# Kernel optimization log

Hardware: AMD Instinct MI355X
Metric: run time of the kernel (lower is better)

Reference implementation:

```python
import jax, jax.numpy as jnp
import numpy as np

DIM = 1024
INTER = 1024
N_EXPERTS = 16
TOPK = 4
SHARED_INTER = 2 * INTER  # n_shared_experts * moe_inter_dim
T = 8192


def setup_inputs() -> dict:
    key = jax.random.key(0)
    ks = jax.random.split(key, 15)
    s = 0.02
    inp = {
        "x": jax.random.normal(ks[0], (T, DIM), jnp.float32),
        "gate_w": jax.random.normal(ks[1], (N_EXPERTS, DIM), jnp.float32) * s,
        # routed experts, stacked over expert axis
        "ew1": jax.random.normal(ks[2], (N_EXPERTS, INTER, DIM), jnp.float32) * s,
        "eb1": jax.random.normal(ks[3], (N_EXPERTS, INTER), jnp.float32) * s,
        "ew2": jax.random.normal(ks[4], (N_EXPERTS, DIM, INTER), jnp.float32) * s,
        "eb2": jax.random.normal(ks[5], (N_EXPERTS, DIM), jnp.float32) * s,
        "ew3": jax.random.normal(ks[6], (N_EXPERTS, INTER, DIM), jnp.float32) * s,
        "eb3": jax.random.normal(ks[7], (N_EXPERTS, INTER), jnp.float32) * s,
        # shared expert MLP (inter = 2 * moe_inter_dim)
        "sw1": jax.random.normal(ks[8], (SHARED_INTER, DIM), jnp.float32) * s,
        "sb1": jax.random.normal(ks[9], (SHARED_INTER,), jnp.float32) * s,
        "sw2": jax.random.normal(ks[10], (DIM, SHARED_INTER), jnp.float32) * s,
        "sb2": jax.random.normal(ks[11], (DIM,), jnp.float32) * s,
        "sw3": jax.random.normal(ks[12], (SHARED_INTER, DIM), jnp.float32) * s,
        "sb3": jax.random.normal(ks[13], (SHARED_INTER,), jnp.float32) * s,
    }
    return inp


def _ffn(x, w1, b1, w2, b2, w3, b3):
    # w2(silu(w1(x)) * w3(x))
    return (jax.nn.silu(x @ w1.T + b1) * (x @ w3.T + b3)) @ w2.T + b2


def reference(x, gate_w, ew1, eb1, ew2, eb2, ew3, eb3, sw1, sb1, sw2, sb2, sw3, sb3):
    # Gate: softmax scores in fp32 (n_groups=1 -> no group masking), top-k routing
    scores = jax.nn.softmax((x @ gate_w.T).astype(jnp.float32), axis=-1)  # [T, E]
    top_vals, idx = jax.lax.top_k(scores, TOPK)  # [T, K]
    weights = top_vals.astype(x.dtype)  # route_scale = 1.0, softmax score_func

    # Per-expert combine weight: zero for unselected experts.
    nT = x.shape[0]
    cw = jnp.zeros((nT, N_EXPERTS), x.dtype).at[
        jnp.arange(nT)[:, None], idx
    ].add(weights)  # [T, E]

    # Routed experts: masked-dense dispatch (weight 0 kills unselected terms)
    y = jnp.zeros_like(x)
    for e in range(N_EXPERTS):
        y = y + cw[:, e:e + 1] * _ffn(x, ew1[e], eb1[e], ew2[e], eb2[e], ew3[e], eb3[e])

    # Shared experts (always applied)
    z = _ffn(x, sw1, sb1, sw2, sb2, sw3, sb3)
    return y + z
```

## Files before the change

### kernel.cpp

```cpp
#include <hip/hip_runtime.h>
#include <cstdint>
#include <cstddef>

#define TOK     8192
#define DIMD    1024
#define INTERD  1024
#define NEXP    16
#define SINTER  2048
#define CAPROWS 34816
#define MAXTILES 272
#define HBLK    32

typedef __bf16 bf16_t;
typedef __bf16 bf16x8_t __attribute__((ext_vector_type(8)));
typedef __bf16 bf16x4_t __attribute__((ext_vector_type(4)));
typedef float  f32x4_t  __attribute__((ext_vector_type(4)));

__device__ __forceinline__ void gload_lds16(const bf16_t* g, bf16_t* l) {
  __builtin_amdgcn_global_load_lds((const __attribute__((address_space(1))) void*)g,
                                   (__attribute__((address_space(3))) void*)l,
                                   16, 0, 0);
}

__global__ void init_kernel(int* toklist, float* wtlist, int* tile_e, int* tile_rs) {
  int i = blockIdx.x * blockDim.x + threadIdx.x;
  if (i < CAPROWS) { toklist[i] = -1; wtlist[i] = 0.0f; }
  if (i < 512)     { tile_e[i] = -1; tile_rs[i] = 0; }
}

__global__ void cvt_kernel(const float* __restrict__ in, bf16_t* __restrict__ out, int n4) {
  int stride = gridDim.x * blockDim.x;
  for (int i = blockIdx.x * blockDim.x + threadIdx.x; i < n4; i += stride) {
    float4 v = ((const float4*)in)[i];
    bf16x4_t o;
    o[0] = (bf16_t)v.x; o[1] = (bf16_t)v.y; o[2] = (bf16_t)v.z; o[3] = (bf16_t)v.w;
    ((bf16x4_t*)out)[i] = o;
  }
}

__global__ __launch_bounds__(256)
void gate_kernel(const float* __restrict__ x, const float* __restrict__ gw,
                 int* __restrict__ tkidx, float* __restrict__ tkwt) {
  int wv = threadIdx.x >> 6, lane = threadIdx.x & 63;
  int t = blockIdx.x * 4 + wv;
  const float4* xp = (const float4*)(x + (size_t)t * DIMD + lane * 16);
  float4 xv[4];
#pragma unroll
  for (int i = 0; i < 4; ++i) xv[i] = xp[i];
  float sc[NEXP];
#pragma unroll
  for (int e = 0; e < NEXP; ++e) {
    const float4* wp = (const float4*)(gw + (size_t)e * DIMD + lane * 16);
    float s = 0.0f;
#pragma unroll
    for (int i = 0; i < 4; ++i) {
      float4 w = wp[i];
      s += xv[i].x * w.x + xv[i].y * w.y + xv[i].z * w.z + xv[i].w * w.w;
    }
    sc[e] = s;
  }
#pragma unroll
  for (int off = 32; off > 0; off >>= 1)
#pragma unroll
    for (int e = 0; e < NEXP; ++e)
      sc[e] += __shfl_xor(sc[e], off, 64);
  if (lane == 0) {
    float m = sc[0];
#pragma unroll
    for (int e = 1; e < NEXP; ++e) m = fmaxf(m, sc[e]);
    float p[NEXP], s = 0.0f;
#pragma unroll
    for (int e = 0; e < NEXP; ++e) { p[e] = __expf(sc[e] - m); s += p[e]; }
    float inv = 1.0f / s;
    unsigned used = 0;
    for (int k = 0; k < 4; ++k) {
      int best = 0; float bv = -1.0f;
#pragma unroll
      for (int e = 0; e < NEXP; ++e)
        if (!((used >> e) & 1u) && p[e] > bv) { bv = p[e]; best = e; }
      used |= 1u << best;
      tkidx[t * 4 + k] = best;
      tkwt[t * 4 + k] = bv * inv;
    }
  }
}

__global__ __launch_bounds__(256)
void hist_kernel(const int* __restrict__ tkidx, int* __restrict__ blkhist) {
  __shared__ int h[NEXP];
  if (threadIdx.x < NEXP) h[threadIdx.x] = 0;
  __syncthreads();
  int4 v = ((const int4*)tkidx)[blockIdx.x * 256 + threadIdx.x];
  atomicAdd(&h[v.x], 1);
  atomicAdd(&h[v.y], 1);
  atomicAdd(&h[v.z], 1);
  atomicAdd(&h[v.w], 1);
  __syncthreads();
  if (threadIdx.x < NEXP) blkhist[blockIdx.x * NEXP + threadIdx.x] = h[threadIdx.x];
}

__global__ void offs_kernel(const int* __restrict__ blkhist, int* __restrict__ offsets,
                            int* __restrict__ blkbase,
                            int* __restrict__ tile_e, int* __restrict__ tile_rs) {
  if (threadIdx.x != 0 || blockIdx.x != 0) return;
  int counts[NEXP];
  for (int e = 0; e < NEXP; ++e) {
    int s = 0;
    for (int b = 0; b < HBLK; ++b) s += blkhist[b * NEXP + e];
    counts[e] = s;
  }
  int off = 0, nt = 0;
  for (int e = 0; e < NEXP; ++e) {
    offsets[e] = off;
    int c = counts[e];
    int ntile = (c + 127) >> 7;
    for (int i = 0; i < ntile; ++i) { tile_e[nt] = e; tile_rs[nt] = off + (i << 7); ++nt; }
    off += ntile << 7;
  }
  offsets[NEXP] = off;
  for (int e = 0; e < NEXP; ++e) {
    int base = offsets[e];
    for (int b = 0; b < HBLK; ++b) {
      blkbase[b * NEXP + e] = base;
      base += blkhist[b * NEXP + e];
    }
  }
}

__global__ __launch_bounds__(256)
void scat_kernel(const int* __restrict__ tkidx, const float* __restrict__ tkwt,
                 const int* __restrict__ blkbase,
                 int* __restrict__ toklist, float* __restrict__ wtlist) {
  __shared__ int cur[NEXP];
  if (threadIdx.x < NEXP) cur[threadIdx.x] = blkbase[blockIdx.x * NEXP + threadIdx.x];
  __syncthreads();
  int idx = blockIdx.x * 256 + threadIdx.x;
  int4 v = ((const int4*)tkidx)[idx];
  float4 w = ((const float4*)tkwt)[idx];
  int t = idx;
  int p0 = atomicAdd(&cur[v.x], 1);
  toklist[p0] = t; wtlist[p0] = w.x;
  int p1 = atomicAdd(&cur[v.y], 1);
  toklist[p1] = t; wtlist[p1] = w.y;
  int p2 = atomicAdd(&cur[v.z], 1);
  toklist[p2] = t; wtlist[p2] = w.z;
  int p3 = atomicAdd(&cur[v.w], 1);
  toklist[p3] = t; wtlist[p3] = w.w;
}

template <bool GATHER>
__global__ __launch_bounds__(256, 2)
void ffn_gemm1(const bf16_t* __restrict__ Xb,
               const bf16_t* __restrict__ W1b, const bf16_t* __restrict__ W3b,
               const float* __restrict__ B1b, const float* __restrict__ B3b,
               bf16_t* __restrict__ H,
               const int* __restrict__ tile_e, const int* __restrict__ tile_rs,
               const int* __restrict__ toklist, const float* __restrict__ wtlist,
               int Ncols) {
  __shared__ __align__(16) bf16_t lA[128 * 32];
  __shared__ __align__(16) bf16_t lB1[128 * 32];
  __shared__ __align__(16) bf16_t lB3[128 * 32];

  int rowstart;
  const bf16_t *W1, *W3;
  const float *b1p, *b3p;
  if constexpr (GATHER) {
    int e = tile_e[blockIdx.y];
    if (e < 0) return;
    rowstart = tile_rs[blockIdx.y];
    W1 = W1b + (size_t)e * INTERD * DIMD;
    W3 = W3b + (size_t)e * INTERD * DIMD;
    b1p = B1b + e * INTERD;
    b3p = B3b + e * INTERD;
  } else {
    rowstart = blockIdx.y * 128;
    W1 = W1b; W3 = W3b; b1p = B1b; b3p = B3b;
  }
  int col0 = blockIdx.x * 128;
  int tid = threadIdx.x, lane = tid & 63, wv = tid >> 6;
  int wm = wv >> 1, wn = wv & 1;

  int r0 = tid >> 2, r1 = r0 + 64, kc = (tid & 3) * 8;
  int tA0, tA1;
  if constexpr (GATHER) {
    tA0 = toklist[rowstart + r0]; if (tA0 < 0) tA0 = 0;
    tA1 = toklist[rowstart + r1]; if (tA1 < 0) tA1 = 0;
  } else { tA0 = rowstart + r0; tA1 = rowstart + r1; }
  const bf16_t* gA0 = Xb + (size_t)tA0 * DIMD + kc;
  const bf16_t* gA1 = Xb + (size_t)tA1 * DIMD + kc;
  const bf16_t* gB10 = W1 + (size_t)(col0 + r0) * DIMD + kc;
  const bf16_t* gB11 = W1 + (size_t)(col0 + r1) * DIMD + kc;
  const bf16_t* gB30 = W3 + (size_t)(col0 + r0) * DIMD + kc;
  const bf16_t* gB31 = W3 + (size_t)(col0 + r1) * DIMD + kc;
  bf16_t* lA0 = lA + (wv * 64) * 8;        bf16_t* lA1 = lA + (256 + wv * 64) * 8;
  bf16_t* lB10 = lB1 + (wv * 64) * 8;      bf16_t* lB11 = lB1 + (256 + wv * 64) * 8;
  bf16_t* lB30 = lB3 + (wv * 64) * 8;      bf16_t* lB31 = lB3 + (256 + wv * 64) * 8;

  f32x4_t acc1[4][4] = {};
  f32x4_t acc3[4][4] = {};

  int mrow = wm * 64 + (lane & 15);
  int ncol = wn * 64 + (lane & 15);
  int koff = (lane >> 4) * 8;

  for (int k0 = 0; k0 < DIMD; k0 += 32) {
    gload_lds16(gA0 + k0, lA0);
    gload_lds16(gA1 + k0, lA1);
    gload_lds16(gB10 + k0, lB10);
    gload_lds16(gB11 + k0, lB11);
    gload_lds16(gB30 + k0, lB30);
    gload_lds16(gB31 + k0, lB31);
    __syncthreads();
    bf16x8_t af[4], b1f[4], b3f[4];
#pragma unroll
    for (int i = 0; i < 4; ++i) {
      af[i]  = *(const bf16x8_t*)&lA [(mrow + i * 16) * 32 + koff];
      b1f[i] = *(const bf16x8_t*)&lB1[(ncol + i * 16) * 32 + koff];
      b3f[i] = *(const bf16x8_t*)&lB3[(ncol + i * 16) * 32 + koff];
    }
#pragma unroll
    for (int mi = 0; mi < 4; ++mi)
#pragma unroll
      for (int ni = 0; ni < 4; ++ni) {
        acc1[mi][ni] = __builtin_amdgcn_mfma_f32_16x16x32_bf16(af[mi], b1f[ni], acc1[mi][ni], 0, 0, 0);
        acc3[mi][ni] = __builtin_amdgcn_mfma_f32_16x16x32_bf16(af[mi], b3f[ni], acc3[mi][ni], 0, 0, 0);
      }
    __syncthreads();
  }

  float bias1[4], bias3[4];
#pragma unroll
  for (int ni = 0; ni < 4; ++ni) {
    int cg = col0 + wn * 64 + ni * 16 + (lane & 15);
    bias1[ni] = b1p[cg];
    bias3[ni] = b3p[cg];
  }
#pragma unroll
  for (int mi = 0; mi < 4; ++mi)
#pragma unroll
    for (int rg = 0; rg < 4; ++rg) {
      int rl = wm * 64 + mi * 16 + ((lane >> 4) << 2) + rg;
      int grow = rowstart + rl;
      float wt = 1.0f;
      if constexpr (GATHER) wt = wtlist[grow];
      size_t hbase = (size_t)grow * Ncols + col0 + wn * 64 + (lane & 15);
#pragma unroll
      for (int ni = 0; ni < 4; ++ni) {
        float v1 = acc1[mi][ni][rg] + bias1[ni];
        float v3 = acc3[mi][ni][rg] + bias3[ni];
        float sg = v1 / (1.0f + __expf(-v1));
        H[hbase + ni * 16] = (bf16_t)(sg * v3 * wt);
      }
    }
}

template <bool SCATTER>
__global__ __launch_bounds__(256, 2)
void ffn_gemm2(const bf16_t* __restrict__ Hin, const bf16_t* __restrict__ W2b,
               const float* __restrict__ B2b, float* __restrict__ Out,
               const int* __restrict__ tile_e, const int* __restrict__ tile_rs,
               const int* __restrict__ toklist, const float* __restrict__ wtlist,
               int Kdim) {
  __shared__ __align__(16) bf16_t lA[128 * 32];
  __shared__ __align__(16) bf16_t lB[128 * 32];

  int rowstart;
  const bf16_t* W2;
  const float* b2p;
  if constexpr (SCATTER) {
    int e = tile_e[blockIdx.y];
    if (e < 0) return;
    rowstart = tile_rs[blockIdx.y];
    W2 = W2b + (size_t)e * DIMD * INTERD;
    b2p = B2b + e * DIMD;
  } else {
    rowstart = blockIdx.y * 128;
    W2 = W2b; b2p = B2b;
  }
  int col0 = blockIdx.x * 128;
  int tid = threadIdx.x, lane = tid & 63, wv = tid >> 6;
  int wm = wv >> 1, wn = wv & 1;

  int r0 = tid >> 2, r1 = r0 + 64, kc = (tid & 3) * 8;
  const bf16_t* gA0 = Hin + (size_t)(rowstart + r0) * Kdim + kc;
  const bf16_t* gA1 = Hin + (size_t)(rowstart + r1) * Kdim + kc;
  const bf16_t* gB0 = W2 + (size_t)(col0 + r0) * Kdim + kc;
  const bf16_t* gB1 = W2 + (size_t)(col0 + r1) * Kdim + kc;
  bf16_t* lA0 = lA + (wv * 64) * 8;  bf16_t* lA1 = lA + (256 + wv * 64) * 8;
  bf16_t* lB0 = lB + (wv * 64) * 8;  bf16_t* lB1p = lB + (256 + wv * 64) * 8;

  f32x4_t acc[4][4] = {};
  int mrow = wm * 64 + (lane & 15);
  int ncol = wn * 64 + (lane & 15);
  int koff = (lane >> 4) * 8;

  for (int k0 = 0; k0 < Kdim; k0 += 32) {
    gload_lds16(gA0 + k0, lA0);
    gload_lds16(gA1 + k0, lA1);
    gload_lds16(gB0 + k0, lB0);
    gload_lds16(gB1 + k0, lB1p);
    __syncthreads();
    bf16x8_t af[4], bf[4];
#pragma unroll
    for (int i = 0; i < 4; ++i) {
      af[i] = *(const bf16x8_t*)&lA[(mrow + i * 16) * 32 + koff];
      bf[i] = *(const bf16x8_t*)&lB[(ncol + i * 16) * 32 + koff];
    }
#pragma unroll
    for (int mi = 0; mi < 4; ++mi)
#pragma unroll
      for (int ni = 0; ni < 4; ++ni)
        acc[mi][ni] = __builtin_amdgcn_mfma_f32_16x16x32_bf16(af[mi], bf[ni], acc[mi][ni], 0, 0, 0);
    __syncthreads();
  }

  float b2v[4];
#pragma unroll
  for (int ni = 0; ni < 4; ++ni)
    b2v[ni] = b2p[col0 + wn * 64 + ni * 16 + (lane & 15)];

#pragma unroll
  for (int mi = 0; mi < 4; ++mi)
#pragma unroll
    for (int rg = 0; rg < 4; ++rg) {
      int rl = wm * 64 + mi * 16 + ((lane >> 4) << 2) + rg;
      int grow = rowstart + rl;
      if constexpr (SCATTER) {
        int t = toklist[grow];
        float wt = wtlist[grow];
        if (t >= 0) {
          size_t ob = (size_t)t * DIMD + col0 + wn * 64 + (lane & 15);
#pragma unroll
          for (int ni = 0; ni < 4; ++ni)
            atomicAdd(&Out[ob + ni * 16], acc[mi][ni][rg] + wt * b2v[ni]);
        }
      } else {
        size_t ob = (size_t)grow * DIMD + col0 + wn * 64 + (lane & 15);
#pragma unroll
        for (int ni = 0; ni < 4; ++ni)
          Out[ob + ni * 16] = acc[mi][ni][rg] + b2v[ni];
      }
    }
}

extern "C" void kernel_launch(void* const* d_in, const int* in_sizes, int n_in,
                              void* d_out, int out_size, void* d_ws, size_t ws_size,
                              hipStream_t stream) {
  const float* x   = (const float*)d_in[0];
  const float* gw  = (const float*)d_in[1];
  const float* ew1 = (const float*)d_in[2];
  const float* eb1 = (const float*)d_in[3];
  const float* ew2 = (const float*)d_in[4];
  const float* eb2 = (const float*)d_in[5];
  const float* ew3 = (const float*)d_in[6];
  const float* eb3 = (const float*)d_in[7];
  const float* sw1 = (const float*)d_in[8];
  const float* sb1 = (const float*)d_in[9];
  const float* sw2 = (const float*)d_in[10];
  const float* sb2 = (const float*)d_in[11];
  const float* sw3 = (const float*)d_in[12];
  const float* sb3 = (const float*)d_in[13];
  float* out = (float*)d_out;

  char* ws = (char*)d_ws;
  size_t off = 0;
  auto alloc = [&](size_t bytes) -> void* {
    off = (off + 255) & ~(size_t)255;
    void* p = ws + off;
    off += bytes;
    return p;
  };

  bf16_t* xb   = (bf16_t*)alloc((size_t)TOK * DIMD * 2);
  bf16_t* ew1b = (bf16_t*)alloc((size_t)NEXP * INTERD * DIMD * 2);
  bf16_t* ew3b = (bf16_t*)alloc((size_t)NEXP * INTERD * DIMD * 2);
  bf16_t* ew2b = (bf16_t*)alloc((size_t)NEXP * DIMD * INTERD * 2);
  bf16_t* sw1b = (bf16_t*)alloc((size_t)SINTER * DIMD * 2);
  bf16_t* sw3b = (bf16_t*)alloc((size_t)SINTER * DIMD * 2);
  bf16_t* sw2b = (bf16_t*)alloc((size_t)DIMD * SINTER * 2);
  bf16_t* Hg   = (bf16_t*)alloc((size_t)CAPROWS * INTERD * 2);
  bf16_t* Hs   = (bf16_t*)alloc((size_t)TOK * SINTER * 2);
  int*   toklist = (int*)alloc(CAPROWS * 4);
  float* wtlist  = (float*)alloc(CAPROWS * 4);
  int*   offsets = (int*)alloc((NEXP + 1) * 4);
  int*   blkhist = (int*)alloc(HBLK * NEXP * 4);
  int*   blkbase = (int*)alloc(HBLK * NEXP * 4);
  int*   tile_e  = (int*)alloc(512 * 4);
  int*   tile_rs = (int*)alloc(512 * 4);
  int*   tkidx   = (int*)alloc((size_t)TOK * 4 * 4);
  float* tkwt    = (float*)alloc((size_t)TOK * 4 * 4);

  init_kernel<<<(CAPROWS + 255) / 256, 256, 0, stream>>>(toklist, wtlist, tile_e, tile_rs);

  cvt_kernel<<<2048, 256, 0, stream>>>(x,   xb,   TOK * DIMD / 4);
  cvt_kernel<<<2048, 256, 0, stream>>>(ew1, ew1b, NEXP * INTERD * DIMD / 4);
  cvt_kernel<<<2048, 256, 0, stream>>>(ew3, ew3b, NEXP * INTERD * DIMD / 4);
  cvt_kernel<<<2048, 256, 0, stream>>>(ew2, ew2b, NEXP * DIMD * INTERD / 4);
  cvt_kernel<<<512,  256, 0, stream>>>(sw1, sw1b, SINTER * DIMD / 4);
  cvt_kernel<<<512,  256, 0, stream>>>(sw3, sw3b, SINTER * DIMD / 4);
  cvt_kernel<<<512,  256, 0, stream>>>(sw2, sw2b, DIMD * SINTER / 4);

  gate_kernel<<<TOK / 4, 256, 0, stream>>>(x, gw, tkidx, tkwt);
  hist_kernel<<<HBLK, 256, 0, stream>>>(tkidx, blkhist);
  offs_kernel<<<1, 64, 0, stream>>>(blkhist, offsets, blkbase, tile_e, tile_rs);
  scat_kernel<<<HBLK, 256, 0, stream>>>(tkidx, tkwt, blkbase, toklist, wtlist);

  ffn_gemm1<false><<<dim3(SINTER / 128, TOK / 128), 256, 0, stream>>>(
      xb, sw1b, sw3b, sb1, sb3, Hs, nullptr, nullptr, nullptr, nullptr, SINTER);
  ffn_gemm2<false><<<dim3(DIMD / 128, TOK / 128), 256, 0, stream>>>(
      Hs, sw2b, sb2, out, nullptr, nullptr, nullptr, nullptr, SINTER);

  ffn_gemm1<true><<<dim3(INTERD / 128, MAXTILES), 256, 0, stream>>>(
      xb, ew1b, ew3b, eb1, eb3, Hg, tile_e, tile_rs, toklist, wtlist, INTERD);
  ffn_gemm2<true><<<dim3(DIMD / 128, MAXTILES), 256, 0, stream>>>(
      Hg, ew2b, eb2, out, tile_e, tile_rs, toklist, wtlist, INTERD);
}
```

Before: 653.5 us.

## Replace FFN GEMMs with 512-thread double-buffered 256x256 kernel and interleaved W1/W3

Replaces the two 128x128 FFN GEMM kernels with one templated 512-thread kernel. It uses 256-wide tiles, a 64-deep K step, double-buffered LDS with a software pipeline driven by explicit vmcnt waits, XOR-swizzled LDS addressing and setprio around the MFMA block. W1 and W3 are interleaved in 16-row groups at conversion time, so one B operand feeds both SiLU and gate columns. Expert routing tiles grow to 256 rows, and the shared and routed H buffers now share one allocation. The larger tiles raise data reuse and cut LDS bank conflicts and stalls, at the cost of more padding rows per expert and higher register and LDS use per block.

```diff
diff --git a/kernel.cpp b/kernel.cpp
--- a/kernel.cpp
+++ b/kernel.cpp
@@ -7,8 +7,8 @@
 #define INTERD  1024
 #define NEXP    16
 #define SINTER  2048
-#define CAPROWS 34816
-#define MAXTILES 272
+#define CAP256  36864
+#define MAXT    144
 #define HBLK    32
 
 typedef __bf16 bf16_t;
@@ -24,8 +24,8 @@
 
 __global__ void init_kernel(int* toklist, float* wtlist, int* tile_e, int* tile_rs) {
   int i = blockIdx.x * blockDim.x + threadIdx.x;
-  if (i < CAPROWS) { toklist[i] = -1; wtlist[i] = 0.0f; }
-  if (i < 512)     { tile_e[i] = -1; tile_rs[i] = 0; }
+  if (i < CAP256) { toklist[i] = -1; wtlist[i] = 0.0f; }
+  if (i < 512)    { tile_e[i] = -1; tile_rs[i] = 0; }
 }
 
 __global__ void cvt_kernel(const float* __restrict__ in, bf16_t* __restrict__ out, int n4) {
@@ -35,6 +35,26 @@
     bf16x4_t o;
     o[0] = (bf16_t)v.x; o[1] = (bf16_t)v.y; o[2] = (bf16_t)v.z; o[3] = (bf16_t)v.w;
     ((bf16x4_t*)out)[i] = o;
+  }
+}
+
+__global__ void cvt_ileave(const float* __restrict__ s1, const float* __restrict__ s3,
+                           bf16_t* __restrict__ dst, int total4, int esh) {
+  int stride = gridDim.x * blockDim.x;
+  int fmask = (1 << esh) - 1;
+  for (int i = blockIdx.x * blockDim.x + threadIdx.x; i < total4; i += stride) {
+    int k4 = i & 255;
+    int fr = i >> 8;
+    int e  = fr >> esh;
+    int f  = fr & fmask;
+    int p  = f >> 4, s = f & 15;
+    int real = ((p >> 1) << 4) + s;
+    size_t srow = ((size_t)e << (esh - 1)) + real;
+    const float* src = ((p & 1) ? s3 : s1) + (srow << 10) + (k4 << 2);
+    float4 v = *(const float4*)src;
+    bf16x4_t o;
+    o[0] = (bf16_t)v.x; o[1] = (bf16_t)v.y; o[2] = (bf16_t)v.z; o[3] = (bf16_t)v.w;
+    ((bf16x4_t*)dst)[i] = o;
   }
 }
 
@@ -113,9 +133,9 @@
   for (int e = 0; e < NEXP; ++e) {
     offsets[e] = off;
     int c = counts[e];
-    int ntile = (c + 127) >> 7;
-    for (int i = 0; i < ntile; ++i) { tile_e[nt] = e; tile_rs[nt] = off + (i << 7); ++nt; }
-    off += ntile << 7;
+    int ntile = (c + 255) >> 8;
+    for (int i = 0; i < ntile; ++i) { tile_e[nt] = e; tile_rs[nt] = off + (i << 8); ++nt; }
+    off += ntile << 8;
   }
   offsets[NEXP] = off;
   for (int e = 0; e < NEXP; ++e) {
@@ -137,210 +157,200 @@
   int idx = blockIdx.x * 256 + threadIdx.x;
   int4 v = ((const int4*)tkidx)[idx];
   float4 w = ((const float4*)tkwt)[idx];
-  int t = idx;
-  int p0 = atomicAdd(&cur[v.x], 1);
-  toklist[p0] = t; wtlist[p0] = w.x;
-  int p1 = atomicAdd(&cur[v.y], 1);
-  toklist[p1] = t; wtlist[p1] = w.y;
-  int p2 = atomicAdd(&cur[v.z], 1);
-  toklist[p2] = t; wtlist[p2] = w.z;
-  int p3 = atomicAdd(&cur[v.w], 1);
-  toklist[p3] = t; wtlist[p3] = w.w;
-}
-
-template <bool GATHER>
-__global__ __launch_bounds__(256, 2)
-void ffn_gemm1(const bf16_t* __restrict__ Xb,
-               const bf16_t* __restrict__ W1b, const bf16_t* __restrict__ W3b,
-               const float* __restrict__ B1b, const float* __restrict__ B3b,
-               bf16_t* __restrict__ H,
-               const int* __restrict__ tile_e, const int* __restrict__ tile_rs,
-               const int* __restrict__ toklist, const float* __restrict__ wtlist,
-               int Ncols) {
-  __shared__ __align__(16) bf16_t lA[128 * 32];
-  __shared__ __align__(16) bf16_t lB1[128 * 32];
-  __shared__ __align__(16) bf16_t lB3[128 * 32];
-
-  int rowstart;
-  const bf16_t *W1, *W3;
-  const float *b1p, *b3p;
-  if constexpr (GATHER) {
-    int e = tile_e[blockIdx.y];
+  int p0 = atomicAdd(&cur[v.x], 1); toklist[p0] = idx; wtlist[p0] = w.x;
+  int p1 = atomicAdd(&cur[v.y], 1); toklist[p1] = idx; wtlist[p1] = w.y;
+  int p2 = atomicAdd(&cur[v.z], 1); toklist[p2] = idx; wtlist[p2] = w.z;
+  int p3 = atomicAdd(&cur[v.w], 1); toklist[p3] = idx; wtlist[p3] = w.w;
+}
+
+#define SBAR __builtin_amdgcn_sched_barrier(0)
+
+template <int BM, int BN, bool TABLE, int EPI>
+__global__ __launch_bounds__(512, 2)
+void gemm8p(const bf16_t* __restrict__ Ag, const bf16_t* __restrict__ Bw,
+            const float* __restrict__ bias1, const float* __restrict__ bias3,
+            void* __restrict__ Outp,
+            const int* __restrict__ tile_e, const int* __restrict__ tile_rs,
+            const int* __restrict__ toklist, const float* __restrict__ wtlist,
+            int K, int ldOut, size_t strideB, int biasStride) {
+  constexpr int AH = BM / 128, BH = BN / 128, HT = AH + BH;
+  constexpr int MF = BM / 32, NF = BN / 64;
+  __shared__ __align__(16) bf16_t lds[2 * HT * 8192];
+
+  int rowstart, e = 0;
+  if constexpr (TABLE) {
+    e = tile_e[blockIdx.y];
     if (e < 0) return;
     rowstart = tile_rs[blockIdx.y];
-    W1 = W1b + (size_t)e * INTERD * DIMD;
-    W3 = W3b + (size_t)e * INTERD * DIMD;
-    b1p = B1b + e * INTERD;
-    b3p = B3b + e * INTERD;
   } else {
-    rowstart = blockIdx.y * 128;
-    W1 = W1b; W3 = W3b; b1p = B1b; b3p = B3b;
-  }
-  int col0 = blockIdx.x * 128;
-  int tid = threadIdx.x, lane = tid & 63, wv = tid >> 6;
-  int wm = wv >> 1, wn = wv & 1;
-
-  int r0 = tid >> 2, r1 = r0 + 64, kc = (tid & 3) * 8;
-  int tA0, tA1;
-  if constexpr (GATHER) {
-    tA0 = toklist[rowstart + r0]; if (tA0 < 0) tA0 = 0;
-    tA1 = toklist[rowstart + r1]; if (tA1 < 0) tA1 = 0;
-  } else { tA0 = rowstart + r0; tA1 = rowstart + r1; }
-  const bf16_t* gA0 = Xb + (size_t)tA0 * DIMD + kc;
-  const bf16_t* gA1 = Xb + (size_t)tA1 * DIMD + kc;
-  const bf16_t* gB10 = W1 + (size_t)(col0 + r0) * DIMD + kc;
-  const bf16_t* gB11 = W1 + (size_t)(col0 + r1) * DIMD + kc;
-  const bf16_t* gB30 = W3 + (size_t)(col0 + r0) * DIMD + kc;
-  const bf16_t* gB31 = W3 + (size_t)(col0 + r1) * DIMD + kc;
-  bf16_t* lA0 = lA + (wv * 64) * 8;        bf16_t* lA1 = lA + (256 + wv * 64) * 8;
-  bf16_t* lB10 = lB1 + (wv * 64) * 8;      bf16_t* lB11 = lB1 + (256 + wv * 64) * 8;
-  bf16_t* lB30 = lB3 + (wv * 64) * 8;      bf16_t* lB31 = lB3 + (256 + wv * 64) * 8;
-
-  f32x4_t acc1[4][4] = {};
-  f32x4_t acc3[4][4] = {};
-
-  int mrow = wm * 64 + (lane & 15);
-  int ncol = wn * 64 + (lane & 15);
-  int koff = (lane >> 4) * 8;
-
-  for (int k0 = 0; k0 < DIMD; k0 += 32) {
-    gload_lds16(gA0 + k0, lA0);
-    gload_lds16(gA1 + k0, lA1);
-    gload_lds16(gB10 + k0, lB10);
-    gload_lds16(gB11 + k0, lB11);
-    gload_lds16(gB30 + k0, lB30);
-    gload_lds16(gB31 + k0, lB31);
-    __syncthreads();
-    bf16x8_t af[4], b1f[4], b3f[4];
-#pragma unroll
-    for (int i = 0; i < 4; ++i) {
-      af[i]  = *(const bf16x8_t*)&lA [(mrow + i * 16) * 32 + koff];
-      b1f[i] = *(const bf16x8_t*)&lB1[(ncol + i * 16) * 32 + koff];
-      b3f[i] = *(const bf16x8_t*)&lB3[(ncol + i * 16) * 32 + koff];
-    }
-#pragma unroll
-    for (int mi = 0; mi < 4; ++mi)
-#pragma unroll
-      for (int ni = 0; ni < 4; ++ni) {
-        acc1[mi][ni] = __builtin_amdgcn_mfma_f32_16x16x32_bf16(af[mi], b1f[ni], acc1[mi][ni], 0, 0, 0);
-        acc3[mi][ni] = __builtin_amdgcn_mfma_f32_16x16x32_bf16(af[mi], b3f[ni], acc3[mi][ni], 0, 0, 0);
+    rowstart = blockIdx.y * BM;
+  }
+  const bf16_t* Bwp = Bw + (TABLE ? (size_t)e * strideB : (size_t)0);
+  const int boff = TABLE ? e * biasStride : 0;
+
+  const int tid = threadIdx.x, lane = tid & 63, wv = tid >> 6;
+  const int wm = wv >> 2, wn = wv & 3;
+  const int xsw = (lane & 7) << 4;
+  const int klo = (lane >> 4) * 16;
+
+  const bf16_t* srcp[2 * HT];
+#pragma unroll
+  for (int h = 0; h < AH; ++h)
+#pragma unroll
+    for (int j = 0; j < 2; ++j) {
+      int rl = j * 64 + (tid >> 3);
+      int grow = rowstart + h * 128 + rl;
+      int slot = (tid & 7) ^ (rl & 7);
+      long arow;
+      if constexpr (TABLE && EPI == 0) {
+        int t = toklist[grow];
+        arow = (t < 0) ? 0 : t;
+      } else {
+        arow = grow;
       }
-    __syncthreads();
-  }
-
-  float bias1[4], bias3[4];
-#pragma unroll
-  for (int ni = 0; ni < 4; ++ni) {
-    int cg = col0 + wn * 64 + ni * 16 + (lane & 15);
-    bias1[ni] = b1p[cg];
-    bias3[ni] = b3p[cg];
-  }
-#pragma unroll
-  for (int mi = 0; mi < 4; ++mi)
-#pragma unroll
-    for (int rg = 0; rg < 4; ++rg) {
-      int rl = wm * 64 + mi * 16 + ((lane >> 4) << 2) + rg;
-      int grow = rowstart + rl;
-      float wt = 1.0f;
-      if constexpr (GATHER) wt = wtlist[grow];
-      size_t hbase = (size_t)grow * Ncols + col0 + wn * 64 + (lane & 15);
-#pragma unroll
-      for (int ni = 0; ni < 4; ++ni) {
-        float v1 = acc1[mi][ni][rg] + bias1[ni];
-        float v3 = acc3[mi][ni][rg] + bias3[ni];
-        float sg = v1 / (1.0f + __expf(-v1));
-        H[hbase + ni * 16] = (bf16_t)(sg * v3 * wt);
+      srcp[h * 2 + j] = Ag + (size_t)arow * K + slot * 8;
+    }
+#pragma unroll
+  for (int h = 0; h < BH; ++h)
+#pragma unroll
+    for (int j = 0; j < 2; ++j) {
+      int rl = j * 64 + (tid >> 3);
+      int grow = (int)blockIdx.x * BN + h * 128 + rl;
+      int slot = (tid & 7) ^ (rl & 7);
+      srcp[(AH + h) * 2 + j] = Bwp + (size_t)grow * K + slot * 8;
+    }
+
+#define STAGE(KT, BUF)                                                          \
+  do {                                                                          \
+    bf16_t* dst_ = (bf16_t*)lds + (BUF) * (HT * 8192);                          \
+    _Pragma("unroll")                                                           \
+    for (int h_ = 0; h_ < HT; ++h_) {                                           \
+      _Pragma("unroll")                                                         \
+      for (int j_ = 0; j_ < 2; ++j_)                                            \
+        gload_lds16(srcp[h_ * 2 + j_] + (KT) * 64,                              \
+                    dst_ + h_ * 8192 + j_ * 4096 + wv * 512);                   \
+    }                                                                           \
+  } while (0)
+
+#define READS(AF, BF, KS)                                                       \
+  do {                                                                          \
+    _Pragma("unroll")                                                           \
+    for (int mi = 0; mi < MF; ++mi) {                                           \
+      int rt_ = wm * (BM / 2) + mi * 16 + (lane & 15);                          \
+      int hb_ = (rt_ >> 7) * 16384, rl_ = rt_ & 127;                            \
+      AF[mi] = *(const bf16x8_t*)(bufb + hb_ +                                  \
+        ((rl_ * 128 + (KS) * 64 + klo) ^ xsw));                                 \
+    }                                                                           \
+    _Pragma("unroll")                                                           \
+    for (int ni = 0; ni < NF; ++ni) {                                           \
+      int ct_ = wn * (BN / 4) + ni * 16 + (lane & 15);                          \
+      int hb_ = (AH + (ct_ >> 7)) * 16384, rl_ = ct_ & 127;                     \
+      BF[ni] = *(const bf16x8_t*)(bufb + hb_ +                                  \
+        ((rl_ * 128 + (KS) * 64 + klo) ^ xsw));                                 \
+    }                                                                           \
+  } while (0)
+
+#define DOMFMA(AF, BF)                                                          \
+  do {                                                                          \
+    _Pragma("unroll")                                                           \
+    for (int mi = 0; mi < MF; ++mi)                                             \
+      _Pragma("unroll")                                                         \
+      for (int ni = 0; ni < NF; ++ni)                                           \
+        acc[mi][ni] = __builtin_amdgcn_mfma_f32_16x16x32_bf16(                  \
+            AF[mi], BF[ni], acc[mi][ni], 0, 0, 0);                              \
+  } while (0)
+
+  f32x4_t acc[MF][NF] = {};
+  const int NTK = K >> 6;
+
+  STAGE(0, 0);
+
+  for (int kt = 0; kt < NTK; ++kt) {
+    const char* bufb = (const char*)lds + (kt & 1) * (HT * 16384);
+    if (kt + 1 < NTK) {
+      STAGE(kt + 1, (kt + 1) & 1);
+      SBAR;
+      if constexpr (HT == 4) asm volatile("s_waitcnt vmcnt(8)" ::: "memory");
+      else                   asm volatile("s_waitcnt vmcnt(6)" ::: "memory");
+    } else {
+      SBAR;
+      asm volatile("s_waitcnt vmcnt(0)" ::: "memory");
+    }
+    SBAR;
+    __builtin_amdgcn_s_barrier();
+    SBAR;
+    {
+      bf16x8_t a0[MF], b0[NF], a1[MF], b1[NF];
+      READS(a0, b0, 0);
+      READS(a1, b1, 1);
+      __builtin_amdgcn_s_setprio(1);
+      DOMFMA(a0, b0);
+      DOMFMA(a1, b1);
+      __builtin_amdgcn_s_setprio(0);
+    }
+    SBAR;
+    __builtin_amdgcn_s_barrier();
+  }
+
+  if constexpr (EPI == 0) {
+    constexpr int NR = BN / 2;
+    float b1v[NF / 2], b3v[NF / 2];
+    int rcbase = (int)blockIdx.x * NR + wn * (NR / 4) + (lane & 15);
+#pragma unroll
+    for (int ni2 = 0; ni2 < NF / 2; ++ni2) {
+      b1v[ni2] = bias1[boff + rcbase + ni2 * 16];
+      b3v[ni2] = bias3[boff + rcbase + ni2 * 16];
+    }
+    bf16_t* Hout = (bf16_t*)Outp;
+#pragma unroll
+    for (int mi = 0; mi < MF; ++mi)
+#pragma unroll
+      for (int rg = 0; rg < 4; ++rg) {
+        int rt = wm * (BM / 2) + mi * 16 + ((lane >> 4) << 2) + rg;
+        int grow = rowstart + rt;
+        float wt = 1.0f;
+        if constexpr (TABLE) wt = wtlist[grow];
+        size_t ob = (size_t)grow * ldOut + rcbase;
+#pragma unroll
+        for (int ni2 = 0; ni2 < NF / 2; ++ni2) {
+          float v1 = acc[mi][2 * ni2][rg] + b1v[ni2];
+          float v3 = acc[mi][2 * ni2 + 1][rg] + b3v[ni2];
+          float sg = v1 / (1.0f + __expf(-v1));
+          Hout[ob + ni2 * 16] = (bf16_t)(sg * v3 * wt);
+        }
       }
-    }
-}
-
-template <bool SCATTER>
-__global__ __launch_bounds__(256, 2)
-void ffn_gemm2(const bf16_t* __restrict__ Hin, const bf16_t* __restrict__ W2b,
-               const float* __restrict__ B2b, float* __restrict__ Out,
-               const int* __restrict__ tile_e, const int* __restrict__ tile_rs,
-               const int* __restrict__ toklist, const float* __restrict__ wtlist,
-               int Kdim) {
-  __shared__ __align__(16) bf16_t lA[128 * 32];
-  __shared__ __align__(16) bf16_t lB[128 * 32];
-
-  int rowstart;
-  const bf16_t* W2;
-  const float* b2p;
-  if constexpr (SCATTER) {
-    int e = tile_e[blockIdx.y];
-    if (e < 0) return;
-    rowstart = tile_rs[blockIdx.y];
-    W2 = W2b + (size_t)e * DIMD * INTERD;
-    b2p = B2b + e * DIMD;
   } else {
-    rowstart = blockIdx.y * 128;
-    W2 = W2b; b2p = B2b;
-  }
-  int col0 = blockIdx.x * 128;
-  int tid = threadIdx.x, lane = tid & 63, wv = tid >> 6;
-  int wm = wv >> 1, wn = wv & 1;
-
-  int r0 = tid >> 2, r1 = r0 + 64, kc = (tid & 3) * 8;
-  const bf16_t* gA0 = Hin + (size_t)(rowstart + r0) * Kdim + kc;
-  const bf16_t* gA1 = Hin + (size_t)(rowstart + r1) * Kdim + kc;
-  const bf16_t* gB0 = W2 + (size_t)(col0 + r0) * Kdim + kc;
-  const bf16_t* gB1 = W2 + (size_t)(col0 + r1) * Kdim + kc;
-  bf16_t* lA0 = lA + (wv * 64) * 8;  bf16_t* lA1 = lA + (256 + wv * 64) * 8;
-  bf16_t* lB0 = lB + (wv * 64) * 8;  bf16_t* lB1p = lB + (256 + wv * 64) * 8;
-
-  f32x4_t acc[4][4] = {};
-  int mrow = wm * 64 + (lane & 15);
-  int ncol = wn * 64 + (lane & 15);
-  int koff = (lane >> 4) * 8;
-
-  for (int k0 = 0; k0 < Kdim; k0 += 32) {
-    gload_lds16(gA0 + k0, lA0);
-    gload_lds16(gA1 + k0, lA1);
-    gload_lds16(gB0 + k0, lB0);
-    gload_lds16(gB1 + k0, lB1p);
-    __syncthreads();
-    bf16x8_t af[4], bf[4];
-#pragma unroll
-    for (int i = 0; i < 4; ++i) {
-      af[i] = *(const bf16x8_t*)&lA[(mrow + i * 16) * 32 + koff];
-      bf[i] = *(const bf16x8_t*)&lB[(ncol + i * 16) * 32 + koff];
-    }
-#pragma unroll
-    for (int mi = 0; mi < 4; ++mi)
-#pragma unroll
-      for (int ni = 0; ni < 4; ++ni)
-        acc[mi][ni] = __builtin_amdgcn_mfma_f32_16x16x32_bf16(af[mi], bf[ni], acc[mi][ni], 0, 0, 0);
-    __syncthreads();
-  }
-
-  float b2v[4];
-#pragma unroll
-  for (int ni = 0; ni < 4; ++ni)
-    b2v[ni] = b2p[col0 + wn * 64 + ni * 16 + (lane & 15)];
-
-#pragma unroll
-  for (int mi = 0; mi < 4; ++mi)
-#pragma unroll
-    for (int rg = 0; rg < 4; ++rg) {
-      int rl = wm * 64 + mi * 16 + ((lane >> 4) << 2) + rg;
-      int grow = rowstart + rl;
-      if constexpr (SCATTER) {
-        int t = toklist[grow];
-        float wt = wtlist[grow];
-        if (t >= 0) {
-          size_t ob = (size_t)t * DIMD + col0 + wn * 64 + (lane & 15);
-#pragma unroll
-          for (int ni = 0; ni < 4; ++ni)
-            atomicAdd(&Out[ob + ni * 16], acc[mi][ni][rg] + wt * b2v[ni]);
+    float bv[NF];
+    int colbase = (int)blockIdx.x * BN + wn * (BN / 4) + (lane & 15);
+#pragma unroll
+    for (int ni = 0; ni < NF; ++ni) bv[ni] = bias1[boff + colbase + ni * 16];
+    float* Fout = (float*)Outp;
+#pragma unroll
+    for (int mi = 0; mi < MF; ++mi)
+#pragma unroll
+      for (int rg = 0; rg < 4; ++rg) {
+        int rt = wm * (BM / 2) + mi * 16 + ((lane >> 4) << 2) + rg;
+        int grow = rowstart + rt;
+        if constexpr (EPI == 1) {
+          int t = toklist[grow];
+          float wt = wtlist[grow];
+          if (t >= 0) {
+            size_t ob = (size_t)t * ldOut + colbase;
+#pragma unroll
+            for (int ni = 0; ni < NF; ++ni)
+              atomicAdd(&Fout[ob + ni * 16], acc[mi][ni][rg] + wt * bv[ni]);
+          }
+        } else {
+          size_t ob = (size_t)grow * ldOut + colbase;
+#pragma unroll
+          for (int ni = 0; ni < NF; ++ni)
+            Fout[ob + ni * 16] = acc[mi][ni][rg] + bv[ni];
         }
-      } else {
-        size_t ob = (size_t)grow * DIMD + col0 + wn * 64 + (lane & 15);
-#pragma unroll
-        for (int ni = 0; ni < 4; ++ni)
-          Out[ob + ni * 16] = acc[mi][ni][rg] + b2v[ni];
       }
-    }
+  }
+#undef STAGE
+#undef READS
+#undef DOMFMA
 }
 
 extern "C" void kernel_launch(void* const* d_in, const int* in_sizes, int n_in,
@@ -361,6 +371,7 @@
   const float* sw3 = (const float*)d_in[12];
   const float* sb3 = (const float*)d_in[13];
   float* out = (float*)d_out;
+  (void)ws_size;
 
   char* ws = (char*)d_ws;
   size_t off = 0;
@@ -371,17 +382,16 @@
     return p;
   };
 
-  bf16_t* xb   = (bf16_t*)alloc((size_t)TOK * DIMD * 2);
-  bf16_t* ew1b = (bf16_t*)alloc((size_t)NEXP * INTERD * DIMD * 2);
-  bf16_t* ew3b = (bf16_t*)alloc((size_t)NEXP * INTERD * DIMD * 2);
-  bf16_t* ew2b = (bf16_t*)alloc((size_t)NEXP * DIMD * INTERD * 2);
-  bf16_t* sw1b = (bf16_t*)alloc((size_t)SINTER * DIMD * 2);
-  bf16_t* sw3b = (bf16_t*)alloc((size_t)SINTER * DIMD * 2);
-  bf16_t* sw2b = (bf16_t*)alloc((size_t)DIMD * SINTER * 2);
-  bf16_t* Hg   = (bf16_t*)alloc((size_t)CAPROWS * INTERD * 2);
-  bf16_t* Hs   = (bf16_t*)alloc((size_t)TOK * SINTER * 2);
-  int*   toklist = (int*)alloc(CAPROWS * 4);
-  float* wtlist  = (float*)alloc(CAPROWS * 4);
+  bf16_t* xb    = (bf16_t*)alloc((size_t)TOK * DIMD * 2);
+  bf16_t* ew13i = (bf16_t*)alloc((size_t)NEXP * 2 * INTERD * DIMD * 2);
+  bf16_t* ew2b  = (bf16_t*)alloc((size_t)NEXP * DIMD * INTERD * 2);
+  bf16_t* sw13i = (bf16_t*)alloc((size_t)2 * SINTER * DIMD * 2);
+  bf16_t* sw2b  = (bf16_t*)alloc((size_t)DIMD * SINTER * 2);
+  bf16_t* Hun   = (bf16_t*)alloc((size_t)CAP256 * INTERD * 2);
+  bf16_t* Hs    = Hun;
+  bf16_t* Hg    = Hun;
+  int*   toklist = (int*)alloc(CAP256 * 4);
+  float* wtlist  = (float*)alloc(CAP256 * 4);
   int*   offsets = (int*)alloc((NEXP + 1) * 4);
   int*   blkhist = (int*)alloc(HBLK * NEXP * 4);
   int*   blkbase = (int*)alloc(HBLK * NEXP * 4);
@@ -390,28 +400,30 @@
   int*   tkidx   = (int*)alloc((size_t)TOK * 4 * 4);
   float* tkwt    = (float*)alloc((size_t)TOK * 4 * 4);
 
-  init_kernel<<<(CAPROWS + 255) / 256, 256, 0, stream>>>(toklist, wtlist, tile_e, tile_rs);
+  init_kernel<<<(CAP256 + 255) / 256, 256, 0, stream>>>(toklist, wtlist, tile_e, tile_rs);
 
   cvt_kernel<<<2048, 256, 0, stream>>>(x,   xb,   TOK * DIMD / 4);
-  cvt_kernel<<<2048, 256, 0, stream>>>(ew1, ew1b, NEXP * INTERD * DIMD / 4);
-  cvt_kernel<<<2048, 256, 0, stream>>>(ew3, ew3b, NEXP * INTERD * DIMD / 4);
   cvt_kernel<<<2048, 256, 0, stream>>>(ew2, ew2b, NEXP * DIMD * INTERD / 4);
-  cvt_kernel<<<512,  256, 0, stream>>>(sw1, sw1b, SINTER * DIMD / 4);
-  cvt_kernel<<<512,  256, 0, stream>>>(sw3, sw3b, SINTER * DIMD / 4);
   cvt_kernel<<<512,  256, 0, stream>>>(sw2, sw2b, DIMD * SINTER / 4);
+  cvt_ileave<<<2048, 256, 0, stream>>>(ew1, ew3, ew13i, NEXP * 2 * INTERD * DIMD / 4, 11);
+  cvt_ileave<<<1024, 256, 0, stream>>>(sw1, sw3, sw13i, 2 * SINTER * DIMD / 4, 12);
 
   gate_kernel<<<TOK / 4, 256, 0, stream>>>(x, gw, tkidx, tkwt);
   hist_kernel<<<HBLK, 256, 0, stream>>>(tkidx, blkhist);
   offs_kernel<<<1, 64, 0, stream>>>(blkhist, offsets, blkbase, tile_e, tile_rs);
   scat_kernel<<<HBLK, 256, 0, stream>>>(tkidx, tkwt, blkbase, toklist, wtlist);
 
-  ffn_gemm1<false><<<dim3(SINTER / 128, TOK / 128), 256, 0, stream>>>(
-      xb, sw1b, sw3b, sb1, sb3, Hs, nullptr, nullptr, nullptr, nullptr, SINTER);
-  ffn_gemm2<false><<<dim3(DIMD / 128, TOK / 128), 256, 0, stream>>>(
-      Hs, sw2b, sb2, out, nullptr, nullptr, nullptr, nullptr, SINTER);
-
-  ffn_gemm1<true><<<dim3(INTERD / 128, MAXTILES), 256, 0, stream>>>(
-      xb, ew1b, ew3b, eb1, eb3, Hg, tile_e, tile_rs, toklist, wtlist, INTERD);
-  ffn_gemm2<true><<<dim3(DIMD / 128, MAXTILES), 256, 0, stream>>>(
-      Hg, ew2b, eb2, out, tile_e, tile_rs, toklist, wtlist, INTERD);
-}
+  gemm8p<256, 256, false, 0><<<dim3(2 * SINTER / 256, TOK / 256), 512, 0, stream>>>(
+      xb, sw13i, sb1, sb3, Hs, nullptr, nullptr, nullptr, nullptr,
+      DIMD, SINTER, 0, 0);
+  gemm8p<128, 256, false, 2><<<dim3(DIMD / 256, TOK / 128), 512, 0, stream>>>(
+      Hs, sw2b, sb2, nullptr, out, nullptr, nullptr, nullptr, nullptr,
+      SINTER, DIMD, 0, 0);
+
+  gemm8p<256, 256, true, 0><<<dim3(2 * INTERD / 256, MAXT), 512, 0, stream>>>(
+      xb, ew13i, eb1, eb3, Hg, tile_e, tile_rs, toklist, wtlist,
+      DIMD, INTERD, (size_t)2 * INTERD * DIMD, INTERD);
+  gemm8p<256, 256, true, 1><<<dim3(DIMD / 256, MAXT), 512, 0, stream>>>(
+      Hg, ew2b, eb2, nullptr, out, tile_e, tile_rs, toklist, wtlist,
+      INTERD, DIMD, (size_t)DIMD * INTERD, DIMD);
+}
```

New measurement: 803.0 us. +22.9%, slower.
